# Kernel optimization log

Hardware: AMD Instinct MI355X
Metric: run time of the kernel (lower is better)

The kernel has to match this reference:

```python
import jax, jax.numpy as jnp
import numpy as np

N_ATOMS = 100000
N_EDGES = 6400000

def setup_inputs() -> dict:
    key = jax.random.key(0)
    k1, k2, k3 = jax.random.split(key, 3)
    R = jax.random.normal(k1, (N_ATOMS, 3), dtype=jnp.float32)
    idx_i = jax.random.randint(k2, (N_EDGES,), 0, N_ATOMS, dtype=jnp.int64)
    idx_j = jax.random.randint(k3, (N_EDGES,), 0, N_ATOMS, dtype=jnp.int64)
    return {"R": R, "idx_i": idx_i, "idx_j": idx_j}

def reference(R, idx_i, idx_j):
    # Gather coordinates at both ends of each edge, subtract, L2 norm over xyz.
    Rij = R[idx_i] - R[idx_j]            # [E, 3]
    d_ij = jnp.sqrt(jnp.sum(Rij * Rij, axis=-1))  # [E]
    return d_ij
```

## Files before the change

kernel.cpp:

```cpp
#include <hip/hip_runtime.h>
#include <hip/hip_bf16.h>


__global__ __launch_bounds__(256) void pairwise_dist_kernel(
    const float* __restrict__ R,
    const int* __restrict__ idx_i,
    const int* __restrict__ idx_j,
    float* __restrict__ out,
    int n_edges)
{
    const int quad = blockIdx.x * blockDim.x + threadIdx.x;
    const int n_quads = n_edges >> 2;

    if (quad < n_quads) {
        const int4 a = ((const int4*)idx_i)[quad];
        const int4 b = ((const int4*)idx_j)[quad];

        float4 o;
        {
            const float* pa = R + 3 * (long)a.x;
            const float* pb = R + 3 * (long)b.x;
            float dx = pa[0] - pb[0], dy = pa[1] - pb[1], dz = pa[2] - pb[2];
            o.x = sqrtf(dx * dx + dy * dy + dz * dz);
        }
        {
            const float* pa = R + 3 * (long)a.y;
            const float* pb = R + 3 * (long)b.y;
            float dx = pa[0] - pb[0], dy = pa[1] - pb[1], dz = pa[2] - pb[2];
            o.y = sqrtf(dx * dx + dy * dy + dz * dz);
        }
        {
            const float* pa = R + 3 * (long)a.z;
            const float* pb = R + 3 * (long)b.z;
            float dx = pa[0] - pb[0], dy = pa[1] - pb[1], dz = pa[2] - pb[2];
            o.z = sqrtf(dx * dx + dy * dy + dz * dz);
        }
        {
            const float* pa = R + 3 * (long)a.w;
            const float* pb = R + 3 * (long)b.w;
            float dx = pa[0] - pb[0], dy = pa[1] - pb[1], dz = pa[2] - pb[2];
            o.w = sqrtf(dx * dx + dy * dy + dz * dz);
        }
        ((float4*)out)[quad] = o;
    }

    const int tail_start = n_quads << 2;
    const int tail = n_edges - tail_start;
    if (tail > 0 && quad < tail) {
        const int e = tail_start + quad;
        const int ia = idx_i[e], ib = idx_j[e];
        const float* pa = R + 3 * (long)ia;
        const float* pb = R + 3 * (long)ib;
        float dx = pa[0] - pb[0], dy = pa[1] - pb[1], dz = pa[2] - pb[2];
        out[e] = sqrtf(dx * dx + dy * dy + dz * dz);
    }
}

extern "C" void kernel_launch(void* const* d_in, const int* in_sizes, int n_in,
                              void* d_out, int out_size, void* d_ws, size_t ws_size,
                              hipStream_t stream)
{
    const float* R     = (const float*)d_in[0];
    const int*   idx_i = (const int*)d_in[1];
    const int*   idx_j = (const int*)d_in[2];
    float*       out   = (float*)d_out;

    const int n_edges = in_sizes[1];
    const int n_quads = (n_edges + 3) >> 2;
    const int block   = 256;
    const int grid    = (n_quads + block - 1) / block;

    pairwise_dist_kernel<<<grid, block, 0, stream>>>(R, idx_i, idx_j, out, n_edges);
}
```

Measured before the change: 144.3 us.

## Pad coordinates to float4 in workspace and gather with vector loads

A pre-pass kernel copies R into a 16-byte-aligned float4 array in the workspace, so each random gather becomes a single 128-bit load instead of three scalar loads. The index loads and output stores switch to nontemporal builtins to keep streaming data from displacing the gathered table in cache. The cost is a second kernel launch plus a 1.6 MB padded copy on every call. The old kernel remains as a fallback when the workspace is too small.

```diff
diff --git a/kernel.cpp b/kernel.cpp
--- a/kernel.cpp
+++ b/kernel.cpp
@@ -1,6 +1,70 @@
 #include <hip/hip_runtime.h>
-#include <hip/hip_bf16.h>
+#include <math.h>
 
+
+typedef int   iv4 __attribute__((ext_vector_type(4)));
+typedef float fv4 __attribute__((ext_vector_type(4)));
+
+__global__ __launch_bounds__(256) void pad_R_kernel(
+    const float* __restrict__ R, fv4* __restrict__ R4, int n_atoms)
+{
+    const int i = blockIdx.x * blockDim.x + threadIdx.x;
+    if (i < n_atoms) {
+        fv4 v;
+        v.x = R[3 * i + 0];
+        v.y = R[3 * i + 1];
+        v.z = R[3 * i + 2];
+        v.w = 0.0f;
+        R4[i] = v;
+    }
+}
+
+__device__ __forceinline__ float edge_dist(fv4 A, fv4 B)
+{
+    const float dx = A.x - B.x, dy = A.y - B.y, dz = A.z - B.z;
+    return sqrtf(dx * dx + dy * dy + dz * dz);
+}
+
+__global__ __launch_bounds__(256) void pairwise_dist4_kernel(
+    const fv4* __restrict__ R4,
+    const int* __restrict__ idx_i,
+    const int* __restrict__ idx_j,
+    float* __restrict__ out,
+    int n_edges)
+{
+    const int quad = blockIdx.x * blockDim.x + threadIdx.x;
+    const int n_quads = n_edges >> 2;
+
+    if (quad < n_quads) {
+        const iv4 a = __builtin_nontemporal_load((const iv4*)idx_i + quad);
+        const iv4 b = __builtin_nontemporal_load((const iv4*)idx_j + quad);
+
+        const fv4 A0 = R4[a.x];
+        const fv4 B0 = R4[b.x];
+        const fv4 A1 = R4[a.y];
+        const fv4 B1 = R4[b.y];
+        const fv4 A2 = R4[a.z];
+        const fv4 B2 = R4[b.z];
+        const fv4 A3 = R4[a.w];
+        const fv4 B3 = R4[b.w];
+
+        fv4 o;
+        o.x = edge_dist(A0, B0);
+        o.y = edge_dist(A1, B1);
+        o.z = edge_dist(A2, B2);
+        o.w = edge_dist(A3, B3);
+        __builtin_nontemporal_store(o, (fv4*)out + quad);
+    }
+
+    const int tail_start = n_quads << 2;
+    const int tail = n_edges - tail_start;
+    if (tail > 0 && quad < tail) {
+        const int e = tail_start + quad;
+        const fv4 A = R4[idx_i[e]];
+        const fv4 B = R4[idx_j[e]];
+        out[e] = edge_dist(A, B);
+    }
+}
 
 __global__ __launch_bounds__(256) void pairwise_dist_kernel(
     const float* __restrict__ R,
@@ -15,7 +79,6 @@
     if (quad < n_quads) {
         const int4 a = ((const int4*)idx_i)[quad];
         const int4 b = ((const int4*)idx_j)[quad];
-
         float4 o;
         {
             const float* pa = R + 3 * (long)a.x;
@@ -66,9 +129,22 @@
     float*       out   = (float*)d_out;
 
     const int n_edges = in_sizes[1];
+
+    const int n0 = in_sizes[0];
+    const int n_atoms = (n0 % 3 == 0) ? n0 / 3 : n0;
+
     const int n_quads = (n_edges + 3) >> 2;
     const int block   = 256;
-    const int grid    = (n_quads + block - 1) / block;
+    int grid = (n_quads + block - 1) / block;
+    if (grid < 1) grid = 1;
 
-    pairwise_dist_kernel<<<grid, block, 0, stream>>>(R, idx_i, idx_j, out, n_edges);
+    const size_t pad_bytes = (size_t)n_atoms * sizeof(fv4);
+    if (d_ws != nullptr && ws_size >= pad_bytes) {
+        fv4* R4 = (fv4*)d_ws;
+        const int pad_grid = (n_atoms + block - 1) / block;
+        pad_R_kernel<<<pad_grid, block, 0, stream>>>(R, R4, n_atoms);
+        pairwise_dist4_kernel<<<grid, block, 0, stream>>>(R4, idx_i, idx_j, out, n_edges);
+    } else {
+        pairwise_dist_kernel<<<grid, block, 0, stream>>>(R, idx_i, idx_j, out, n_edges);
+    }
 }
```

Result: slower. 152.0 us (+5.3%).
